# Performance work log

Hardware: AMD Instinct MI355X
Metric: run time of the kernel (lower is better)

Reference implementation:

```python
import jax, jax.numpy as jnp
import numpy as np
from jax import lax

DT = 0.1
V_DES = 12.64798288
T_HW = 0.50284384
A_MAX = 0.10033688
B_SAFE = 4.98937183
DELTA = 1.0
S0 = 0.13082412

B, S, I, H, K = 2048, 128, 8, 256, 50


def _lstm_layer(x, Wih, Whh, bih, bhh):
    # x: (B, S, in). PyTorch gate order: i, f, g, o. Fold both biases once.
    Bn = x.shape[0]
    Hd = Whh.shape[1]
    xg = jnp.einsum('bsi,gi->bsg', x, Wih) + bih + bhh  # (B, S, 4H)

    def step(carry, xg_t):
        h, c = carry
        g = xg_t + h @ Whh.T
        i, f, gg, o = jnp.split(g, 4, axis=-1)
        c = jax.nn.sigmoid(f) * c + jax.nn.sigmoid(i) * jnp.tanh(gg)
        h = jax.nn.sigmoid(o) * jnp.tanh(c)
        return (h, c), h

    init = (jnp.zeros((Bn, Hd), x.dtype), jnp.zeros((Bn, Hd), x.dtype))
    _, hs = lax.scan(step, init, jnp.swapaxes(xg, 0, 1))
    return jnp.swapaxes(hs, 0, 1)  # (B, S, H)


def _idm_rollout(v0, s_gap0, v_lead, horizon):
    sqrt_ab = float(np.sqrt(max(A_MAX, 1e-6) * max(B_SAFE, 1e-6)))

    def step(carry, _):
        v, s = carry
        dv = v_lead - v
        s_c = jnp.maximum(s, 1e-6)
        s_star = jnp.maximum(S0 + v * T_HW + v * dv / (2.0 * sqrt_ab + 1e-6), 0.0)
        acc = A_MAX * (1.0 - (v / V_DES) ** DELTA - (s_star / s_c) ** 2)
        v_next = jnp.maximum(v + DT * acc, 0.0)
        s_next = jnp.maximum(s + dv * DT, 1e-6)
        return (v_next, s_next), v_next

    _, vs = lax.scan(step, (v0, s_gap0), None, length=horizon)
    return jnp.swapaxes(vs, 0, 1)  # (B, K)


def setup_inputs() -> dict:
    key = jax.random.key(0)
    ks = jax.random.split(key, 14)
    sc = 0.05
    x = jax.random.uniform(ks[0], (B, S, I), jnp.float32) * 12.0  # speeds/features in [0, 12] m/s
    s_safe = 1.0 + jax.random.uniform(ks[1], (B,), jnp.float32) * 49.0  # gap in [1, 50] m
    v_lead = jax.random.uniform(ks[2], (B,), jnp.float32) * 12.0
    return {
        'x': x,
        's_safe_initial': s_safe,
        'v_lead_initial': v_lead,
        'Wih0': jax.random.normal(ks[3], (4 * H, I), jnp.float32) * sc,
        'Whh0': jax.random.normal(ks[4], (4 * H, H), jnp.float32) * sc,
        'bih0': jax.random.normal(ks[5], (4 * H,), jnp.float32) * sc,
        'bhh0': jax.random.normal(ks[6], (4 * H,), jnp.float32) * sc,
        'Wih1': jax.random.normal(ks[7], (4 * H, H), jnp.float32) * sc,
        'Whh1': jax.random.normal(ks[8], (4 * H, H), jnp.float32) * sc,
        'bih1': jax.random.normal(ks[9], (4 * H,), jnp.float32) * sc,
        'bhh1': jax.random.normal(ks[10], (4 * H,), jnp.float32) * sc,
        'Wfc': jax.random.normal(ks[11], (K, H), jnp.float32) * sc,
        'bfc': jax.random.normal(ks[12], (K,), jnp.float32) * sc,
    }


def reference(x, s_safe_initial, v_lead_initial, Wih0, Whh0, bih0, bhh0,
              Wih1, Whh1, bih1, bhh1, Wfc, bfc):
    h = _lstm_layer(x, Wih0, Whh0, bih0, bhh0)
    h = _lstm_layer(h, Wih1, Whh1, bih1, bhh1)
    y_lstm = h[:, -1, :] @ Wfc.T + bfc  # (B, K)
    y_idm = _idm_rollout(x[:, -1, 0], s_safe_initial, v_lead_initial, Wfc.shape[0])
    return (y_lstm, y_idm)
```

## Files before the change

kernel.cpp:

```cpp
#include <hip/hip_runtime.h>
#include <stdint.h>

typedef float f32x4 __attribute__((ext_vector_type(4)));
typedef unsigned int uint;
typedef unsigned long long ull;

#define NB 2048
#define NS 128
#define NI 8
#define NH 256
#define NG 1024
#define NK 50

#define A_SC 16.0f
#define W_SC 32.0f
#define INV_SC (1.0f/(A_SC*W_SC))

#define DT_    0.1f
#define V_DES_ 12.64798288f
#define T_HW_  0.50284384f
#define A_MAX_ 0.10033688f
#define B_SAFE_ 4.98937183f
#define S0_    0.13082412f

#define HADDR(row, boff) (((row) << 8) + (((((boff) >> 3) ^ ((row) & 15)) & 31) << 3) + ((boff) & 7))
#define GIDX(row, col) (((row) << 8) + ((col) ^ (((row) & 12) << 2)))

__device__ __forceinline__ uint8_t f2fp8(float v) {
    int r = __builtin_amdgcn_cvt_pk_fp8_f32(v, v, 0, false);
    return (uint8_t)(r & 0xff);
}
__device__ __forceinline__ float sigm(float x) { return 1.0f / (1.0f + __expf(-x)); }
__device__ __forceinline__ float tanh_f(float x) {
    x = fminf(fmaxf(x, -15.0f), 15.0f);
    float e = __expf(2.0f * x);
    return (e - 1.0f) / (e + 1.0f);
}

__global__ void k_pack(const float* __restrict__ W, uint8_t* __restrict__ out,
                       int tiles, int KB, int Nsrc, int Ksrc) {
    int gid = blockIdx.x * 256 + threadIdx.x;
    int total = tiles * KB * 64;
    if (gid >= total) return;
    int lane = gid & 63;
    int kb   = (gid >> 6) % KB;
    int tile = gid / (64 * KB);
    int n = tile * 16 + (lane & 15);
    int kbase = kb * 32 + (lane >> 4) * 8;
    uint64_t wbits = 0;
    #pragma unroll
    for (int j = 0; j < 8; ++j) {
        int k = kbase + j;
        float v = (n < Nsrc && k < Ksrc) ? W[(size_t)n * Ksrc + k] * W_SC : 0.0f;
        wbits |= ((uint64_t)f2fp8(v)) << (8 * j);
    }
    *(uint64_t*)(out + (size_t)gid * 8) = wbits;
}

__global__ void k_bias(const float* __restrict__ bih0, const float* __restrict__ bhh0,
                       const float* __restrict__ bih1, const float* __restrict__ bhh1,
                       float* __restrict__ b0, float* __restrict__ b1) {
    int i = blockIdx.x * 256 + threadIdx.x;
    if (i < NG) b0[i] = bih0[i] + bhh0[i];
    else if (i < 2 * NG) b1[i - NG] = bih1[i - NG] + bhh1[i - NG];
}

__global__ void k_x8(const float* __restrict__ x, uint8_t* __restrict__ x8) {
    int i = blockIdx.x * 256 + threadIdx.x;
    if (i < NB * NS * NI) x8[i] = f2fp8(x[i] * A_SC);
}

__global__ __launch_bounds__(512, 2)
void k_lstm3(const uint8_t* __restrict__ x8,
             const uint8_t* __restrict__ Wih0P, const uint8_t* __restrict__ Whh0P,
             const uint8_t* __restrict__ Wih1P, const uint8_t* __restrict__ Whh1P,
             const uint8_t* __restrict__ WfcP,
             const float* __restrict__ bias0, const float* __restrict__ bias1,
             const float* __restrict__ bfc,
             uint8_t* __restrict__ h0g, uint8_t* __restrict__ h1g,
             uint* __restrict__ ctrs, float* __restrict__ out) {
    __shared__ uint8_t h0st[8192];
    __shared__ uint8_t h1st[8192];
    __shared__ float gA[8192];
    __shared__ float gB[8192];

    const int tid  = threadIdx.x;
    const int w    = tid >> 6, lane = tid & 63;
    const int lrow = lane & 15, kgrp = lane >> 4;
    const int blk  = blockIdx.x;
    const int grp  = blk >> 2, slc = blk & 3;
    const int rowbase = grp * 32;
    const int g = w & 3, ub = w >> 1 & 0;
    const int ubk = w >> 2;

    long wI0[2], wH0[2][8], wI1[2][8], wH1[2][8];
    #pragma unroll
    for (int cc = 0; cc < 2; ++cc) {
        int T = g * 16 + slc * 4 + ubk * 2 + cc;
        wI0[cc] = *(const long*)(Wih0P + ((size_t)T * 64 + lane) * 8);
        #pragma unroll
        for (int kb = 0; kb < 8; ++kb) {
            wH0[cc][kb] = *(const long*)(Whh0P + (((size_t)T * 8 + kb) * 64 + lane) * 8);
            wI1[cc][kb] = *(const long*)(Wih1P + (((size_t)T * 8 + kb) * 64 + lane) * 8);
            wH1[cc][kb] = *(const long*)(Whh1P + (((size_t)T * 8 + kb) * 64 + lane) * 8);
        }
    }

    const int uu = tid & 63;
    const int rb = (tid >> 6) * 4;
    float bs0[4], bs1[4];
    #pragma unroll
    for (int q = 0; q < 4; ++q) {
        int n = q * 256 + slc * 64 + uu;
        bs0[q] = bias0[n]; bs1[q] = bias1[n];
    }
    float c0v[4] = {0,0,0,0}, c1v[4] = {0,0,0,0};

    { int4 z = {0,0,0,0}; ((int4*)h0st)[tid] = z; ((int4*)h1st)[tid] = z; }
    __syncthreads();

    uint8_t* const h0base = h0g + (size_t)grp * 16384;
    uint8_t* const h1base = h1g + (size_t)grp * 16384;
    uint* const myctr = ctrs + grp * 16;
    uint tgt = 0;

    for (int p = 0; p <= NS; ++p) {
        if (p < NS) {
            f32x4 acc[2][2];
            #pragma unroll
            for (int rr = 0; rr < 2; ++rr) { acc[rr][0] = (f32x4){0,0,0,0}; acc[rr][1] = (f32x4){0,0,0,0}; }
            #pragma unroll
            for (int rr = 0; rr < 2; ++rr) {
                long a0 = 0;
                if (kgrp == 0) a0 = *(const long*)(x8 + (size_t)(rowbase + rr * 16 + lrow) * (NS * NI) + p * 8);
                acc[rr][0] = __builtin_amdgcn_mfma_f32_16x16x32_fp8_fp8(a0, wI0[0], acc[rr][0], 0, 0, 0);
                acc[rr][1] = __builtin_amdgcn_mfma_f32_16x16x32_fp8_fp8(a0, wI0[1], acc[rr][1], 0, 0, 0);
                #pragma unroll
                for (int kb = 0; kb < 8; ++kb) {
                    long af = *(const long*)&h0st[HADDR(rr * 16 + lrow, kb * 32 + kgrp * 8)];
                    acc[rr][0] = __builtin_amdgcn_mfma_f32_16x16x32_fp8_fp8(af, wH0[0][kb], acc[rr][0], 0, 0, 0);
                    acc[rr][1] = __builtin_amdgcn_mfma_f32_16x16x32_fp8_fp8(af, wH0[1][kb], acc[rr][1], 0, 0, 0);
                }
            }
            #pragma unroll
            for (int rr = 0; rr < 2; ++rr)
            #pragma unroll
            for (int cc = 0; cc < 2; ++cc) {
                int colb = g * 64 + ubk * 32 + cc * 16 + lrow;
                #pragma unroll
                for (int r = 0; r < 4; ++r)
                    gA[GIDX(rr * 16 + kgrp * 4 + r, colb)] = acc[rr][cc][r];
            }
        }
        __syncthreads();

        if (p < NS) {
            uint8_t* dst = h0base + (size_t)(p & 1) * 8192;
            #pragma unroll
            for (int r = 0; r < 4; ++r) {
                int row = rb + r;
                float iv = gA[GIDX(row, uu)]       * INV_SC + bs0[0];
                float fv = gA[GIDX(row, 64 + uu)]  * INV_SC + bs0[1];
                float gv = gA[GIDX(row, 128 + uu)] * INV_SC + bs0[2];
                float ov = gA[GIDX(row, 192 + uu)] * INV_SC + bs0[3];
                float c = sigm(fv) * c0v[r] + sigm(iv) * tanh_f(gv);
                c0v[r] = c;
                float h = sigm(ov) * tanh_f(c);
                __hip_atomic_store(dst + row * 256 + slc * 64 + uu, f2fp8(h * A_SC),
                                   __ATOMIC_RELAXED, __HIP_MEMORY_SCOPE_AGENT);
            }
        }

        if (p >= 1) {
            f32x4 acc1[2][2];
            #pragma unroll
            for (int rr = 0; rr < 2; ++rr) { acc1[rr][0] = (f32x4){0,0,0,0}; acc1[rr][1] = (f32x4){0,0,0,0}; }
            #pragma unroll
            for (int rr = 0; rr < 2; ++rr) {
                #pragma unroll
                for (int kb = 0; kb < 8; ++kb) {
                    long af0 = *(const long*)&h0st[HADDR(rr * 16 + lrow, kb * 32 + kgrp * 8)];
                    acc1[rr][0] = __builtin_amdgcn_mfma_f32_16x16x32_fp8_fp8(af0, wI1[0][kb], acc1[rr][0], 0, 0, 0);
                    acc1[rr][1] = __builtin_amdgcn_mfma_f32_16x16x32_fp8_fp8(af0, wI1[1][kb], acc1[rr][1], 0, 0, 0);
                    long af1 = *(const long*)&h1st[HADDR(rr * 16 + lrow, kb * 32 + kgrp * 8)];
                    acc1[rr][0] = __builtin_amdgcn_mfma_f32_16x16x32_fp8_fp8(af1, wH1[0][kb], acc1[rr][0], 0, 0, 0);
                    acc1[rr][1] = __builtin_amdgcn_mfma_f32_16x16x32_fp8_fp8(af1, wH1[1][kb], acc1[rr][1], 0, 0, 0);
                }
            }
            #pragma unroll
            for (int rr = 0; rr < 2; ++rr)
            #pragma unroll
            for (int cc = 0; cc < 2; ++cc) {
                int colb = g * 64 + ubk * 32 + cc * 16 + lrow;
                #pragma unroll
                for (int r = 0; r < 4; ++r)
                    gB[GIDX(rr * 16 + kgrp * 4 + r, colb)] = acc1[rr][cc][r];
            }
        }
        __syncthreads();

        if (p >= 1) {
            uint8_t* dst = h1base + (size_t)((p - 1) & 1) * 8192;
            #pragma unroll
            for (int r = 0; r < 4; ++r) {
                int row = rb + r;
                float iv = gB[GIDX(row, uu)]       * INV_SC + bs1[0];
                float fv = gB[GIDX(row, 64 + uu)]  * INV_SC + bs1[1];
                float gv = gB[GIDX(row, 128 + uu)] * INV_SC + bs1[2];
                float ov = gB[GIDX(row, 192 + uu)] * INV_SC + bs1[3];
                float c = sigm(fv) * c1v[r] + sigm(iv) * tanh_f(gv);
                c1v[r] = c;
                float h = sigm(ov) * tanh_f(c);
                __hip_atomic_store(dst + row * 256 + slc * 64 + uu, f2fp8(h * A_SC),
                                   __ATOMIC_RELAXED, __HIP_MEMORY_SCOPE_AGENT);
            }
        }
        __syncthreads();

        tgt += 4;
        if (tid == 0) {
            __hip_atomic_fetch_add(myctr, 1u, __ATOMIC_RELAXED, __HIP_MEMORY_SCOPE_AGENT);
            int gd = 0;
            while (__hip_atomic_load(myctr, __ATOMIC_RELAXED, __HIP_MEMORY_SCOPE_AGENT) < tgt) {
                __builtin_amdgcn_s_sleep(1);
                if (++gd >= (1 << 22)) break;
            }
        }
        __syncthreads();

        {
            int rrow = tid & 31, seg = tid >> 5;
            const ull* s0p = (const ull*)(h0base + (size_t)(p & 1) * 8192 + rrow * 256 + seg * 16);
            const ull* s1p = (const ull*)(h1base + (size_t)((p + 1) & 1) * 8192 + rrow * 256 + seg * 16);
            #pragma unroll
            for (int j = 0; j < 2; ++j) {
                ull q0 = __hip_atomic_load(s0p + j, __ATOMIC_RELAXED, __HIP_MEMORY_SCOPE_AGENT);
                ull q1 = __hip_atomic_load(s1p + j, __ATOMIC_RELAXED, __HIP_MEMORY_SCOPE_AGENT);
                *(ull*)&h0st[HADDR(rrow, seg * 16 + j * 8)] = q0;
                *(ull*)&h1st[HADDR(rrow, seg * 16 + j * 8)] = q1;
            }
        }
        __syncthreads();
    }

    if (w < 2) {
        f32x4 a = (f32x4){0,0,0,0};
        #pragma unroll
        for (int kb = 0; kb < 8; ++kb) {
            long af = *(const long*)&h1st[HADDR(w * 16 + lrow, kb * 32 + kgrp * 8)];
            long bf = *(const long*)(WfcP + (((size_t)slc * 8 + kb) * 64 + lane) * 8);
            a = __builtin_amdgcn_mfma_f32_16x16x32_fp8_fp8(af, bf, a, 0, 0, 0);
        }
        int col = slc * 16 + lrow;
        if (col < NK) {
            float bb = bfc[col];
            #pragma unroll
            for (int r = 0; r < 4; ++r) {
                int row = rowbase + w * 16 + kgrp * 4 + r;
                out[(size_t)row * NK + col] = a[r] * INV_SC + bb;
            }
        }
    }
}

__global__ void k_idm(const float* __restrict__ x, const float* __restrict__ s0,
                      const float* __restrict__ vl, float* __restrict__ out) {
    int b = blockIdx.x * 256 + threadIdx.x;
    if (b >= NB) return;
    float v = x[(size_t)b * NS * NI + (NS - 1) * NI + 0];
    float s = s0[b];
    float vlead = vl[b];
    const float den = 2.0f * sqrtf(A_MAX_ * B_SAFE_) + 1e-6f;
    float* o = out + (size_t)NB * NK + (size_t)b * NK;
    #pragma unroll 1
    for (int k = 0; k < NK; ++k) {
        float dv = vlead - v;
        float sc = fmaxf(s, 1e-6f);
        float ss = fmaxf(S0_ + v * T_HW_ + v * dv / den, 0.0f);
        float a = A_MAX_ * (1.0f - v / V_DES_ - (ss / sc) * (ss / sc));
        v = fmaxf(v + DT_ * a, 0.0f);
        s = fmaxf(s + dv * DT_, 1e-6f);
        o[k] = v;
    }
}

extern "C" void kernel_launch(void* const* d_in, const int* in_sizes, int n_in,
                              void* d_out, int out_size, void* d_ws, size_t ws_size,
                              hipStream_t stream) {
    const float* x    = (const float*)d_in[0];
    const float* s0   = (const float*)d_in[1];
    const float* vl   = (const float*)d_in[2];
    const float* Wih0 = (const float*)d_in[3];
    const float* Whh0 = (const float*)d_in[4];
    const float* bih0 = (const float*)d_in[5];
    const float* bhh0 = (const float*)d_in[6];
    const float* Wih1 = (const float*)d_in[7];
    const float* Whh1 = (const float*)d_in[8];
    const float* bih1 = (const float*)d_in[9];
    const float* bhh1 = (const float*)d_in[10];
    const float* Wfc  = (const float*)d_in[11];
    const float* bfc  = (const float*)d_in[12];
    float* out = (float*)d_out;

    uint8_t* ws = (uint8_t*)d_ws;
    size_t off = 0;
    auto alloc = [&](size_t n) { uint8_t* p = ws + off; off += (n + 255) & ~(size_t)255; return p; };
    uint8_t* Wih0P = alloc(64 * 1 * 64 * 8);
    uint8_t* Whh0P = alloc(64 * 8 * 64 * 8);
    uint8_t* Wih1P = alloc(64 * 8 * 64 * 8);
    uint8_t* Whh1P = alloc(64 * 8 * 64 * 8);
    uint8_t* WfcP  = alloc(4 * 8 * 64 * 8);
    float* b0 = (float*)alloc(NG * 4);
    float* b1 = (float*)alloc(NG * 4);
    uint8_t* x8 = alloc((size_t)NB * NS * NI);
    uint8_t* h0g = alloc((size_t)64 * 16384);
    uint8_t* h1g = alloc((size_t)64 * 16384);
    uint*    ctrs = (uint*)alloc(64 * 64);
    size_t hz = (size_t)(((uint8_t*)ctrs + 64 * 64) - h0g);

    k_pack<<<(64 * 1 * 64 + 255) / 256, 256, 0, stream>>>(Wih0, Wih0P, 64, 1, NG, NI);
    k_pack<<<(64 * 8 * 64 + 255) / 256, 256, 0, stream>>>(Whh0, Whh0P, 64, 8, NG, NH);
    k_pack<<<(64 * 8 * 64 + 255) / 256, 256, 0, stream>>>(Wih1, Wih1P, 64, 8, NG, NH);
    k_pack<<<(64 * 8 * 64 + 255) / 256, 256, 0, stream>>>(Whh1, Whh1P, 64, 8, NG, NH);
    k_pack<<<(4 * 8 * 64 + 255) / 256, 256, 0, stream>>>(Wfc, WfcP, 4, 8, NK, NH);
    k_bias<<<(2 * NG + 255) / 256, 256, 0, stream>>>(bih0, bhh0, bih1, bhh1, b0, b1);
    k_x8<<<(NB * NS * NI + 255) / 256, 256, 0, stream>>>(x, x8);
    hipMemsetAsync(h0g, 0, hz, stream);

    void* kargs[] = { (void*)&x8, (void*)&Wih0P, (void*)&Whh0P, (void*)&Wih1P, (void*)&Whh1P,
                      (void*)&WfcP, (void*)&b0, (void*)&b1, (void*)&bfc,
                      (void*)&h0g, (void*)&h1g, (void*)&ctrs, (void*)&out };
    hipError_t ce = hipLaunchCooperativeKernel((const void*)k_lstm3, dim3(256), dim3(512), kargs, 0, stream);
    if (ce != hipSuccess) {
        k_lstm3<<<256, 512, 0, stream>>>(x8, Wih0P, Whh0P, Wih1P, Whh1P, WfcP, b0, b1, bfc, h0g, h1g, ctrs, out);
    }
    k_idm<<<(NB + 255) / 256, 256, 0, stream>>>(x, s0, vl, out);
}
```

Before: 924.1 us.

## Split each LSTM row group across eight blocks instead of four

Each 32-row batch group is now handled by 8 cooperating blocks, each owning 32 hidden units instead of 64. This halves per-block MFMA work, weight registers and gate LDS, and allows 4 blocks per CU with 512 total blocks. The bias is pre-scaled and folded into the accumulator store, and the gate stage packs two fp8 outputs per store. The cost is more blocks participating in each per-step counter barrier, and higher occupancy that may pressure registers.

```diff
diff --git a/kernel.cpp b/kernel.cpp
--- a/kernel.cpp
+++ b/kernel.cpp
@@ -4,6 +4,7 @@
 typedef float f32x4 __attribute__((ext_vector_type(4)));
 typedef unsigned int uint;
 typedef unsigned long long ull;
+typedef unsigned short ushort_t;
 
 #define NB 2048
 #define NS 128
@@ -14,6 +15,7 @@
 
 #define A_SC 16.0f
 #define W_SC 32.0f
+#define SC_PROD 512.0f
 #define INV_SC (1.0f/(A_SC*W_SC))
 
 #define DT_    0.1f
@@ -24,7 +26,7 @@
 #define S0_    0.13082412f
 
 #define HADDR(row, boff) (((row) << 8) + (((((boff) >> 3) ^ ((row) & 15)) & 31) << 3) + ((boff) & 7))
-#define GIDX(row, col) (((row) << 8) + ((col) ^ (((row) & 12) << 2)))
+#define GIDX(row, col) (((row) << 7) + ((col) ^ (((row) & 12) << 2)))
 
 __device__ __forceinline__ uint8_t f2fp8(float v) {
     int r = __builtin_amdgcn_cvt_pk_fp8_f32(v, v, 0, false);
@@ -61,8 +63,8 @@
                        const float* __restrict__ bih1, const float* __restrict__ bhh1,
                        float* __restrict__ b0, float* __restrict__ b1) {
     int i = blockIdx.x * 256 + threadIdx.x;
-    if (i < NG) b0[i] = bih0[i] + bhh0[i];
-    else if (i < 2 * NG) b1[i - NG] = bih1[i - NG] + bhh1[i - NG];
+    if (i < NG) b0[i] = (bih0[i] + bhh0[i]) * SC_PROD;
+    else if (i < 2 * NG) b1[i - NG] = (bih1[i - NG] + bhh1[i - NG]) * SC_PROD;
 }
 
 __global__ void k_x8(const float* __restrict__ x, uint8_t* __restrict__ x8) {
@@ -70,8 +72,8 @@
     if (i < NB * NS * NI) x8[i] = f2fp8(x[i] * A_SC);
 }
 
-__global__ __launch_bounds__(512, 2)
-void k_lstm3(const uint8_t* __restrict__ x8,
+__global__ __launch_bounds__(512, 4)
+void k_lstm4(const uint8_t* __restrict__ x8,
              const uint8_t* __restrict__ Wih0P, const uint8_t* __restrict__ Whh0P,
              const uint8_t* __restrict__ Wih1P, const uint8_t* __restrict__ Whh1P,
              const uint8_t* __restrict__ WfcP,
@@ -81,44 +83,43 @@
              uint* __restrict__ ctrs, float* __restrict__ out) {
     __shared__ uint8_t h0st[8192];
     __shared__ uint8_t h1st[8192];
-    __shared__ float gA[8192];
-    __shared__ float gB[8192];
+    __shared__ float gA[4096];
+    __shared__ float gB[4096];
 
     const int tid  = threadIdx.x;
     const int w    = tid >> 6, lane = tid & 63;
     const int lrow = lane & 15, kgrp = lane >> 4;
     const int blk  = blockIdx.x;
-    const int grp  = blk >> 2, slc = blk & 3;
+    const int grp  = blk >> 3, slc = blk & 7;
     const int rowbase = grp * 32;
-    const int g = w & 3, ub = w >> 1 & 0;
-    const int ubk = w >> 2;
-
-    long wI0[2], wH0[2][8], wI1[2][8], wH1[2][8];
+    const int g = w & 3, uh = w >> 2;
+    const int T = g * 16 + slc * 2 + uh;
+
+    long wI0, wH0[8], wI1[8], wH1[8];
+    wI0 = *(const long*)(Wih0P + ((size_t)T * 64 + lane) * 8);
     #pragma unroll
-    for (int cc = 0; cc < 2; ++cc) {
-        int T = g * 16 + slc * 4 + ubk * 2 + cc;
-        wI0[cc] = *(const long*)(Wih0P + ((size_t)T * 64 + lane) * 8);
-        #pragma unroll
-        for (int kb = 0; kb < 8; ++kb) {
-            wH0[cc][kb] = *(const long*)(Whh0P + (((size_t)T * 8 + kb) * 64 + lane) * 8);
-            wI1[cc][kb] = *(const long*)(Wih1P + (((size_t)T * 8 + kb) * 64 + lane) * 8);
-            wH1[cc][kb] = *(const long*)(Whh1P + (((size_t)T * 8 + kb) * 64 + lane) * 8);
-        }
-    }
-
-    const int uu = tid & 63;
-    const int rb = (tid >> 6) * 4;
-    float bs0[4], bs1[4];
+    for (int kb = 0; kb < 8; ++kb) {
+        wH0[kb] = *(const long*)(Whh0P + (((size_t)T * 8 + kb) * 64 + lane) * 8);
+        wI1[kb] = *(const long*)(Wih1P + (((size_t)T * 8 + kb) * 64 + lane) * 8);
+        wH1[kb] = *(const long*)(Whh1P + (((size_t)T * 8 + kb) * 64 + lane) * 8);
+    }
+    asm volatile("" : "+v"(wI0));
     #pragma unroll
-    for (int q = 0; q < 4; ++q) {
-        int n = q * 256 + slc * 64 + uu;
-        bs0[q] = bias0[n]; bs1[q] = bias1[n];
-    }
-    float c0v[4] = {0,0,0,0}, c1v[4] = {0,0,0,0};
+    for (int kb = 0; kb < 8; ++kb)
+        asm volatile("" : "+v"(wH0[kb]), "+v"(wI1[kb]), "+v"(wH1[kb]));
+
+    const int colw = g * 32 + uh * 16 + lrow;
+    const float bw0 = bias0[g * 256 + slc * 32 + uh * 16 + lrow];
+    const float bw1 = bias1[g * 256 + slc * 32 + uh * 16 + lrow];
+
+    const int nrow = tid >> 4;
+    const int nu2  = (tid & 15) * 2;
+    float c0v[2] = {0, 0}, c1v[2] = {0, 0};
 
     { int4 z = {0,0,0,0}; ((int4*)h0st)[tid] = z; ((int4*)h1st)[tid] = z; }
     __syncthreads();
 
+    const int abase = HADDR(lrow, kgrp * 8);
     uint8_t* const h0base = h0g + (size_t)grp * 16384;
     uint8_t* const h1base = h1g + (size_t)grp * 16384;
     uint* const myctr = ctrs + grp * 16;
@@ -126,98 +127,96 @@
 
     for (int p = 0; p <= NS; ++p) {
         if (p < NS) {
-            f32x4 acc[2][2];
-            #pragma unroll
-            for (int rr = 0; rr < 2; ++rr) { acc[rr][0] = (f32x4){0,0,0,0}; acc[rr][1] = (f32x4){0,0,0,0}; }
+            f32x4 acc[2];
+            acc[0] = (f32x4){0,0,0,0}; acc[1] = (f32x4){0,0,0,0};
             #pragma unroll
             for (int rr = 0; rr < 2; ++rr) {
                 long a0 = 0;
                 if (kgrp == 0) a0 = *(const long*)(x8 + (size_t)(rowbase + rr * 16 + lrow) * (NS * NI) + p * 8);
-                acc[rr][0] = __builtin_amdgcn_mfma_f32_16x16x32_fp8_fp8(a0, wI0[0], acc[rr][0], 0, 0, 0);
-                acc[rr][1] = __builtin_amdgcn_mfma_f32_16x16x32_fp8_fp8(a0, wI0[1], acc[rr][1], 0, 0, 0);
+                acc[rr] = __builtin_amdgcn_mfma_f32_16x16x32_fp8_fp8(a0, wI0, acc[rr], 0, 0, 0);
                 #pragma unroll
                 for (int kb = 0; kb < 8; ++kb) {
-                    long af = *(const long*)&h0st[HADDR(rr * 16 + lrow, kb * 32 + kgrp * 8)];
-                    acc[rr][0] = __builtin_amdgcn_mfma_f32_16x16x32_fp8_fp8(af, wH0[0][kb], acc[rr][0], 0, 0, 0);
-                    acc[rr][1] = __builtin_amdgcn_mfma_f32_16x16x32_fp8_fp8(af, wH0[1][kb], acc[rr][1], 0, 0, 0);
+                    long af = *(const long*)&h0st[(abase + rr * 4096) ^ (kb << 5)];
+                    acc[rr] = __builtin_amdgcn_mfma_f32_16x16x32_fp8_fp8(af, wH0[kb], acc[rr], 0, 0, 0);
                 }
             }
             #pragma unroll
             for (int rr = 0; rr < 2; ++rr)
             #pragma unroll
-            for (int cc = 0; cc < 2; ++cc) {
-                int colb = g * 64 + ubk * 32 + cc * 16 + lrow;
-                #pragma unroll
-                for (int r = 0; r < 4; ++r)
-                    gA[GIDX(rr * 16 + kgrp * 4 + r, colb)] = acc[rr][cc][r];
+            for (int r = 0; r < 4; ++r) {
+                int row = rr * 16 + kgrp * 4 + r;
+                gA[GIDX(row, colw)] = acc[rr][r] + bw0;
             }
         }
         __syncthreads();
 
         if (p < NS) {
-            uint8_t* dst = h0base + (size_t)(p & 1) * 8192;
-            #pragma unroll
-            for (int r = 0; r < 4; ++r) {
-                int row = rb + r;
-                float iv = gA[GIDX(row, uu)]       * INV_SC + bs0[0];
-                float fv = gA[GIDX(row, 64 + uu)]  * INV_SC + bs0[1];
-                float gv = gA[GIDX(row, 128 + uu)] * INV_SC + bs0[2];
-                float ov = gA[GIDX(row, 192 + uu)] * INV_SC + bs0[3];
-                float c = sigm(fv) * c0v[r] + sigm(iv) * tanh_f(gv);
-                c0v[r] = c;
-                float h = sigm(ov) * tanh_f(c);
-                __hip_atomic_store(dst + row * 256 + slc * 64 + uu, f2fp8(h * A_SC),
-                                   __ATOMIC_RELAXED, __HIP_MEMORY_SCOPE_AGENT);
-            }
+            float2 gq[4];
+            #pragma unroll
+            for (int q = 0; q < 4; ++q)
+                gq[q] = *(float2*)&gA[GIDX(nrow, q * 32 + nu2)];
+            float hh[2];
+            #pragma unroll
+            for (int u = 0; u < 2; ++u) {
+                float iv = ((u ? gq[0].y : gq[0].x)) * INV_SC;
+                float fv = ((u ? gq[1].y : gq[1].x)) * INV_SC;
+                float gv = ((u ? gq[2].y : gq[2].x)) * INV_SC;
+                float ov = ((u ? gq[3].y : gq[3].x)) * INV_SC;
+                float c = sigm(fv) * c0v[u] + sigm(iv) * tanh_f(gv);
+                c0v[u] = c;
+                hh[u] = sigm(ov) * tanh_f(c);
+            }
+            int pk = __builtin_amdgcn_cvt_pk_fp8_f32(hh[0] * A_SC, hh[1] * A_SC, 0, false);
+            __hip_atomic_store((ushort_t*)(h0base + (size_t)(p & 1) * 8192 + nrow * 256 + slc * 32 + nu2),
+                               (ushort_t)(pk & 0xffff), __ATOMIC_RELAXED, __HIP_MEMORY_SCOPE_AGENT);
         }
 
         if (p >= 1) {
-            f32x4 acc1[2][2];
-            #pragma unroll
-            for (int rr = 0; rr < 2; ++rr) { acc1[rr][0] = (f32x4){0,0,0,0}; acc1[rr][1] = (f32x4){0,0,0,0}; }
+            f32x4 acc[2];
+            acc[0] = (f32x4){0,0,0,0}; acc[1] = (f32x4){0,0,0,0};
             #pragma unroll
             for (int rr = 0; rr < 2; ++rr) {
                 #pragma unroll
                 for (int kb = 0; kb < 8; ++kb) {
-                    long af0 = *(const long*)&h0st[HADDR(rr * 16 + lrow, kb * 32 + kgrp * 8)];
-                    acc1[rr][0] = __builtin_amdgcn_mfma_f32_16x16x32_fp8_fp8(af0, wI1[0][kb], acc1[rr][0], 0, 0, 0);
-                    acc1[rr][1] = __builtin_amdgcn_mfma_f32_16x16x32_fp8_fp8(af0, wI1[1][kb], acc1[rr][1], 0, 0, 0);
-                    long af1 = *(const long*)&h1st[HADDR(rr * 16 + lrow, kb * 32 + kgrp * 8)];
-                    acc1[rr][0] = __builtin_amdgcn_mfma_f32_16x16x32_fp8_fp8(af1, wH1[0][kb], acc1[rr][0], 0, 0, 0);
-                    acc1[rr][1] = __builtin_amdgcn_mfma_f32_16x16x32_fp8_fp8(af1, wH1[1][kb], acc1[rr][1], 0, 0, 0);
+                    long af0 = *(const long*)&h0st[(abase + rr * 4096) ^ (kb << 5)];
+                    acc[rr] = __builtin_amdgcn_mfma_f32_16x16x32_fp8_fp8(af0, wI1[kb], acc[rr], 0, 0, 0);
+                    long af1 = *(const long*)&h1st[(abase + rr * 4096) ^ (kb << 5)];
+                    acc[rr] = __builtin_amdgcn_mfma_f32_16x16x32_fp8_fp8(af1, wH1[kb], acc[rr], 0, 0, 0);
                 }
             }
             #pragma unroll
             for (int rr = 0; rr < 2; ++rr)
             #pragma unroll
-            for (int cc = 0; cc < 2; ++cc) {
-                int colb = g * 64 + ubk * 32 + cc * 16 + lrow;
-                #pragma unroll
-                for (int r = 0; r < 4; ++r)
-                    gB[GIDX(rr * 16 + kgrp * 4 + r, colb)] = acc1[rr][cc][r];
+            for (int r = 0; r < 4; ++r) {
+                int row = rr * 16 + kgrp * 4 + r;
+                gB[GIDX(row, colw)] = acc[rr][r] + bw1;
             }
         }
         __syncthreads();
 
         if (p >= 1) {
-            uint8_t* dst = h1base + (size_t)((p - 1) & 1) * 8192;
-            #pragma unroll
-            for (int r = 0; r < 4; ++r) {
-                int row = rb + r;
-                float iv = gB[GIDX(row, uu)]       * INV_SC + bs1[0];
-                float fv = gB[GIDX(row, 64 + uu)]  * INV_SC + bs1[1];
-                float gv = gB[GIDX(row, 128 + uu)] * INV_SC + bs1[2];
-                float ov = gB[GIDX(row, 192 + uu)] * INV_SC + bs1[3];
-                float c = sigm(fv) * c1v[r] + sigm(iv) * tanh_f(gv);
-                c1v[r] = c;
-                float h = sigm(ov) * tanh_f(c);
-                __hip_atomic_store(dst + row * 256 + slc * 64 + uu, f2fp8(h * A_SC),
-                                   __ATOMIC_RELAXED, __HIP_MEMORY_SCOPE_AGENT);
-            }
-        }
-        __syncthreads();
-
-        tgt += 4;
+            float2 gq[4];
+            #pragma unroll
+            for (int q = 0; q < 4; ++q)
+                gq[q] = *(float2*)&gB[GIDX(nrow, q * 32 + nu2)];
+            float hh[2];
+            #pragma unroll
+            for (int u = 0; u < 2; ++u) {
+                float iv = ((u ? gq[0].y : gq[0].x)) * INV_SC;
+                float fv = ((u ? gq[1].y : gq[1].x)) * INV_SC;
+                float gv = ((u ? gq[2].y : gq[2].x)) * INV_SC;
+                float ov = ((u ? gq[3].y : gq[3].x)) * INV_SC;
+                float c = sigm(fv) * c1v[u] + sigm(iv) * tanh_f(gv);
+                c1v[u] = c;
+                hh[u] = sigm(ov) * tanh_f(c);
+            }
+            int pk = __builtin_amdgcn_cvt_pk_fp8_f32(hh[0] * A_SC, hh[1] * A_SC, 0, false);
+            __hip_atomic_store((ushort_t*)(h1base + (size_t)((p - 1) & 1) * 8192 + nrow * 256 + slc * 32 + nu2),
+                               (ushort_t)(pk & 0xffff), __ATOMIC_RELAXED, __HIP_MEMORY_SCOPE_AGENT);
+        }
+        __syncthreads();
+
+        tgt += 8;
         if (tid == 0) {
             __hip_atomic_fetch_add(myctr, 1u, __ATOMIC_RELAXED, __HIP_MEMORY_SCOPE_AGENT);
             int gd = 0;
@@ -243,7 +242,7 @@
         __syncthreads();
     }
 
-    if (w < 2) {
+    if (slc < 4 && w < 2) {
         f32x4 a = (f32x4){0,0,0,0};
         #pragma unroll
         for (int kb = 0; kb < 8; ++kb) {
@@ -330,9 +329,9 @@
     void* kargs[] = { (void*)&x8, (void*)&Wih0P, (void*)&Whh0P, (void*)&Wih1P, (void*)&Whh1P,
                       (void*)&WfcP, (void*)&b0, (void*)&b1, (void*)&bfc,
                       (void*)&h0g, (void*)&h1g, (void*)&ctrs, (void*)&out };
-    hipError_t ce = hipLaunchCooperativeKernel((const void*)k_lstm3, dim3(256), dim3(512), kargs, 0, stream);
+    hipError_t ce = hipLaunchCooperativeKernel((const void*)k_lstm4, dim3(512), dim3(512), kargs, 0, stream);
     if (ce != hipSuccess) {
-        k_lstm3<<<256, 512, 0, stream>>>(x8, Wih0P, Whh0P, Wih1P, Whh1P, WfcP, b0, b1, bfc, h0g, h1g, ctrs, out);
+        k_lstm4<<<512, 512, 0, stream>>>(x8, Wih0P, Whh0P, Wih1P, Whh1P, WfcP, b0, b1, bfc, h0g, h1g, ctrs, out);
     }
     k_idm<<<(NB + 255) / 256, 256, 0, stream>>>(x, s0, vl, out);
 }
```

New measurement: 1.051 ms. 13.7% more time.

## Split per-layer inter-block counters and overlap layer-1 hidden exchange with compute

Applied to the files above, without the earlier changes.

Replaces the single end-of-step counter barrier with separate counters for layer-0 and layer-1 hidden states, so each block waits only for the data it needs and the layer-1 exchange is prefetched at the start of the next step. It also vectorises the gate epilogue (float4 reads, packed fp8 stores of four units), uses 16-byte LDS reads with a new swizzle, folds the pre-scaled bias into the accumulator writeback, and pins weights in AGPRs via inline asm. The intent is to cut inter-block synchronisation latency and LDS/global traffic on each recurrent step, at the cost of more complex ordering that could introduce races.

```diff
diff --git a/kernel.cpp b/kernel.cpp
--- a/kernel.cpp
+++ b/kernel.cpp
@@ -2,6 +2,7 @@
 #include <stdint.h>
 
 typedef float f32x4 __attribute__((ext_vector_type(4)));
+typedef long long2_t __attribute__((ext_vector_type(2)));
 typedef unsigned int uint;
 typedef unsigned long long ull;
 
@@ -14,7 +15,8 @@
 
 #define A_SC 16.0f
 #define W_SC 32.0f
-#define INV_SC (1.0f/(A_SC*W_SC))
+#define SC_PROD 512.0f
+#define INV_SC (1.0f/512.0f)
 
 #define DT_    0.1f
 #define V_DES_ 12.64798288f
@@ -23,7 +25,7 @@
 #define B_SAFE_ 4.98937183f
 #define S0_    0.13082412f
 
-#define HADDR(row, boff) (((row) << 8) + (((((boff) >> 3) ^ ((row) & 15)) & 31) << 3) + ((boff) & 7))
+#define HADDR16(row, boff) (((row) << 8) + (((((boff) >> 4) ^ ((row) & 15)) & 15) << 4) + ((boff) & 15))
 #define GIDX(row, col) (((row) << 8) + ((col) ^ (((row) & 12) << 2)))
 
 __device__ __forceinline__ uint8_t f2fp8(float v) {
@@ -61,8 +63,8 @@
                        const float* __restrict__ bih1, const float* __restrict__ bhh1,
                        float* __restrict__ b0, float* __restrict__ b1) {
     int i = blockIdx.x * 256 + threadIdx.x;
-    if (i < NG) b0[i] = bih0[i] + bhh0[i];
-    else if (i < 2 * NG) b1[i - NG] = bih1[i - NG] + bhh1[i - NG];
+    if (i < NG) b0[i] = (bih0[i] + bhh0[i]) * SC_PROD;
+    else if (i < 2 * NG) b1[i - NG] = (bih1[i - NG] + bhh1[i - NG]) * SC_PROD;
 }
 
 __global__ void k_x8(const float* __restrict__ x, uint8_t* __restrict__ x8) {
@@ -71,7 +73,7 @@
 }
 
 __global__ __launch_bounds__(512, 2)
-void k_lstm3(const uint8_t* __restrict__ x8,
+void k_lstm6(const uint8_t* __restrict__ x8,
              const uint8_t* __restrict__ Wih0P, const uint8_t* __restrict__ Whh0P,
              const uint8_t* __restrict__ Wih1P, const uint8_t* __restrict__ Whh1P,
              const uint8_t* __restrict__ WfcP,
@@ -85,13 +87,11 @@
     __shared__ float gB[8192];
 
     const int tid  = threadIdx.x;
-    const int w    = tid >> 6, lane = tid & 63;
+    const int lane = tid & 63, w = tid >> 6;
     const int lrow = lane & 15, kgrp = lane >> 4;
-    const int blk  = blockIdx.x;
-    const int grp  = blk >> 2, slc = blk & 3;
+    const int grp  = blockIdx.x >> 2, slc = blockIdx.x & 3;
     const int rowbase = grp * 32;
-    const int g = w & 3, ub = w >> 1 & 0;
-    const int ubk = w >> 2;
+    const int g = w & 3, ubk = w >> 2;
 
     long wI0[2], wH0[2][8], wI1[2][8], wH1[2][8];
     #pragma unroll
@@ -105,162 +105,212 @@
             wH1[cc][kb] = *(const long*)(Whh1P + (((size_t)T * 8 + kb) * 64 + lane) * 8);
         }
     }
-
-    const int uu = tid & 63;
-    const int rb = (tid >> 6) * 4;
-    float bs0[4], bs1[4];
     #pragma unroll
-    for (int q = 0; q < 4; ++q) {
-        int n = q * 256 + slc * 64 + uu;
-        bs0[q] = bias0[n]; bs1[q] = bias1[n];
-    }
+    for (int cc = 0; cc < 2; ++cc) {
+        asm volatile("" : "+a"(wI0[cc]));
+        #pragma unroll
+        for (int kb = 0; kb < 8; ++kb)
+            asm volatile("" : "+a"(wH0[cc][kb]), "+a"(wI1[cc][kb]), "+a"(wH1[cc][kb]));
+    }
+
+    float bw0[2], bw1[2];
+    #pragma unroll
+    for (int cc = 0; cc < 2; ++cc) {
+        int n = g * 256 + slc * 64 + ubk * 32 + cc * 16 + lrow;
+        bw0[cc] = bias0[n]; bw1[cc] = bias1[n];
+    }
+
+    const int nrow = tid >> 4;
+    const int ub4  = (tid & 15) * 4;
     float c0v[4] = {0,0,0,0}, c1v[4] = {0,0,0,0};
 
     { int4 z = {0,0,0,0}; ((int4*)h0st)[tid] = z; ((int4*)h1st)[tid] = z; }
     __syncthreads();
 
-    uint8_t* const h0base = h0g + (size_t)grp * 16384;
-    uint8_t* const h1base = h1g + (size_t)grp * 16384;
-    uint* const myctr = ctrs + grp * 16;
-    uint tgt = 0;
+    uint8_t* const h0gg = h0g + (size_t)grp * 16384;
+    uint8_t* const h1gg = h1g + (size_t)grp * 16384;
+    uint* const ctr0 = ctrs + grp * 32;
+    uint* const ctr1 = ctrs + grp * 32 + 16;
+    uint t0 = 0, t1 = 0;
+
+    const int rrow = tid & 31, seg = tid >> 5;
+    const int rkb = seg >> 1, rkg = (seg & 1) << 1;
+    const int rboff0 = rkg * 64 + rkb * 8, rboff1 = (rkg + 1) * 64 + rkb * 8;
+
+#define WAITC(CP, TGT) do { \
+    if (tid == 0) { \
+        uint gd_ = 0; \
+        while (__hip_atomic_load((CP), __ATOMIC_RELAXED, __HIP_MEMORY_SCOPE_AGENT) < (TGT)) { \
+            __builtin_amdgcn_s_sleep(1); \
+            if (++gd_ > (1u << 24)) break; \
+        } \
+    } \
+    __syncthreads(); \
+} while (0)
 
     for (int p = 0; p <= NS; ++p) {
+        ull pr0 = 0, pr1 = 0;
+        if (p >= 2) {
+            WAITC(ctr1, t1);
+            const uint8_t* s = h1gg + (size_t)(p & 1) * 8192 + rrow * 256 + seg * 16;
+            pr0 = __hip_atomic_load((const ull*)s,       __ATOMIC_RELAXED, __HIP_MEMORY_SCOPE_AGENT);
+            pr1 = __hip_atomic_load((const ull*)(s + 8), __ATOMIC_RELAXED, __HIP_MEMORY_SCOPE_AGENT);
+        }
+
         if (p < NS) {
             f32x4 acc[2][2];
             #pragma unroll
             for (int rr = 0; rr < 2; ++rr) { acc[rr][0] = (f32x4){0,0,0,0}; acc[rr][1] = (f32x4){0,0,0,0}; }
             #pragma unroll
             for (int rr = 0; rr < 2; ++rr) {
-                long a0 = 0;
-                if (kgrp == 0) a0 = *(const long*)(x8 + (size_t)(rowbase + rr * 16 + lrow) * (NS * NI) + p * 8);
-                acc[rr][0] = __builtin_amdgcn_mfma_f32_16x16x32_fp8_fp8(a0, wI0[0], acc[rr][0], 0, 0, 0);
-                acc[rr][1] = __builtin_amdgcn_mfma_f32_16x16x32_fp8_fp8(a0, wI0[1], acc[rr][1], 0, 0, 0);
+                long ax = 0;
+                if (kgrp == 0) ax = *(const long*)(x8 + (size_t)(rowbase + rr * 16 + lrow) * (NS * NI) + p * 8);
+                acc[rr][0] = __builtin_amdgcn_mfma_f32_16x16x32_fp8_fp8(ax, wI0[0], acc[rr][0], 0, 0, 0);
+                acc[rr][1] = __builtin_amdgcn_mfma_f32_16x16x32_fp8_fp8(ax, wI0[1], acc[rr][1], 0, 0, 0);
                 #pragma unroll
-                for (int kb = 0; kb < 8; ++kb) {
-                    long af = *(const long*)&h0st[HADDR(rr * 16 + lrow, kb * 32 + kgrp * 8)];
-                    acc[rr][0] = __builtin_amdgcn_mfma_f32_16x16x32_fp8_fp8(af, wH0[0][kb], acc[rr][0], 0, 0, 0);
-                    acc[rr][1] = __builtin_amdgcn_mfma_f32_16x16x32_fp8_fp8(af, wH0[1][kb], acc[rr][1], 0, 0, 0);
+                for (int kbh = 0; kbh < 4; ++kbh) {
+                    const int gsw = ((((kgrp << 2) + kbh) ^ lrow) & 15) << 4;
+                    long2_t q = *(const long2_t*)&h0st[((rr * 16 + lrow) << 8) + gsw];
+                    acc[rr][0] = __builtin_amdgcn_mfma_f32_16x16x32_fp8_fp8(q.x, wH0[0][2*kbh],   acc[rr][0], 0, 0, 0);
+                    acc[rr][0] = __builtin_amdgcn_mfma_f32_16x16x32_fp8_fp8(q.y, wH0[0][2*kbh+1], acc[rr][0], 0, 0, 0);
+                    acc[rr][1] = __builtin_amdgcn_mfma_f32_16x16x32_fp8_fp8(q.x, wH0[1][2*kbh],   acc[rr][1], 0, 0, 0);
+                    acc[rr][1] = __builtin_amdgcn_mfma_f32_16x16x32_fp8_fp8(q.y, wH0[1][2*kbh+1], acc[rr][1], 0, 0, 0);
                 }
             }
             #pragma unroll
             for (int rr = 0; rr < 2; ++rr)
             #pragma unroll
             for (int cc = 0; cc < 2; ++cc) {
-                int colb = g * 64 + ubk * 32 + cc * 16 + lrow;
+                const int colw = g * 64 + ubk * 32 + cc * 16 + lrow;
                 #pragma unroll
                 for (int r = 0; r < 4; ++r)
-                    gA[GIDX(rr * 16 + kgrp * 4 + r, colb)] = acc[rr][cc][r];
+                    gA[GIDX(rr * 16 + kgrp * 4 + r, colw)] = acc[rr][cc][r] + bw0[cc];
             }
         }
         __syncthreads();
 
         if (p < NS) {
-            uint8_t* dst = h0base + (size_t)(p & 1) * 8192;
-            #pragma unroll
-            for (int r = 0; r < 4; ++r) {
-                int row = rb + r;
-                float iv = gA[GIDX(row, uu)]       * INV_SC + bs0[0];
-                float fv = gA[GIDX(row, 64 + uu)]  * INV_SC + bs0[1];
-                float gv = gA[GIDX(row, 128 + uu)] * INV_SC + bs0[2];
-                float ov = gA[GIDX(row, 192 + uu)] * INV_SC + bs0[3];
-                float c = sigm(fv) * c0v[r] + sigm(iv) * tanh_f(gv);
-                c0v[r] = c;
-                float h = sigm(ov) * tanh_f(c);
-                __hip_atomic_store(dst + row * 256 + slc * 64 + uu, f2fp8(h * A_SC),
-                                   __ATOMIC_RELAXED, __HIP_MEMORY_SCOPE_AGENT);
-            }
-        }
+            float4 q0 = *(float4*)&gA[GIDX(nrow, ub4)];
+            float4 q1 = *(float4*)&gA[GIDX(nrow, 64 + ub4)];
+            float4 q2 = *(float4*)&gA[GIDX(nrow, 128 + ub4)];
+            float4 q3 = *(float4*)&gA[GIDX(nrow, 192 + ub4)];
+            float hh[4];
+            #pragma unroll
+            for (int u = 0; u < 4; ++u) {
+                float iv = (&q0.x)[u] * INV_SC, fv = (&q1.x)[u] * INV_SC;
+                float gv = (&q2.x)[u] * INV_SC, ov = (&q3.x)[u] * INV_SC;
+                float c = sigm(fv) * c0v[u] + sigm(iv) * tanh_f(gv);
+                c0v[u] = c;
+                hh[u] = sigm(ov) * tanh_f(c) * A_SC;
+            }
+            int pk = __builtin_amdgcn_cvt_pk_fp8_f32(hh[0], hh[1], 0, false);
+            pk = __builtin_amdgcn_cvt_pk_fp8_f32(hh[2], hh[3], pk, true);
+            __hip_atomic_store((uint*)(h0gg + (size_t)(p & 1) * 8192 + nrow * 256 + slc * 64 + ub4),
+                               (uint)pk, __ATOMIC_RELAXED, __HIP_MEMORY_SCOPE_AGENT);
+        }
+        if (p >= 2) {
+            *(ull*)&h1st[HADDR16(rrow, rboff0)] = pr0;
+            *(ull*)&h1st[HADDR16(rrow, rboff1)] = pr1;
+        }
+        __syncthreads();
+        if (p < NS) { if (tid == 0) __hip_atomic_fetch_add(ctr0, 1u, __ATOMIC_RELAXED, __HIP_MEMORY_SCOPE_AGENT); t0 += 4; }
 
         if (p >= 1) {
-            f32x4 acc1[2][2];
-            #pragma unroll
-            for (int rr = 0; rr < 2; ++rr) { acc1[rr][0] = (f32x4){0,0,0,0}; acc1[rr][1] = (f32x4){0,0,0,0}; }
+            f32x4 acc[2][2];
+            #pragma unroll
+            for (int rr = 0; rr < 2; ++rr) { acc[rr][0] = (f32x4){0,0,0,0}; acc[rr][1] = (f32x4){0,0,0,0}; }
             #pragma unroll
             for (int rr = 0; rr < 2; ++rr) {
                 #pragma unroll
-                for (int kb = 0; kb < 8; ++kb) {
-                    long af0 = *(const long*)&h0st[HADDR(rr * 16 + lrow, kb * 32 + kgrp * 8)];
-                    acc1[rr][0] = __builtin_amdgcn_mfma_f32_16x16x32_fp8_fp8(af0, wI1[0][kb], acc1[rr][0], 0, 0, 0);
-                    acc1[rr][1] = __builtin_amdgcn_mfma_f32_16x16x32_fp8_fp8(af0, wI1[1][kb], acc1[rr][1], 0, 0, 0);
-                    long af1 = *(const long*)&h1st[HADDR(rr * 16 + lrow, kb * 32 + kgrp * 8)];
-                    acc1[rr][0] = __builtin_amdgcn_mfma_f32_16x16x32_fp8_fp8(af1, wH1[0][kb], acc1[rr][0], 0, 0, 0);
-                    acc1[rr][1] = __builtin_amdgcn_mfma_f32_16x16x32_fp8_fp8(af1, wH1[1][kb], acc1[rr][1], 0, 0, 0);
+                for (int kbh = 0; kbh < 4; ++kbh) {
+                    const int gsw = ((((kgrp << 2) + kbh) ^ lrow) & 15) << 4;
+                    long2_t q = *(const long2_t*)&h0st[((rr * 16 + lrow) << 8) + gsw];
+                    long2_t r2 = *(const long2_t*)&h1st[((rr * 16 + lrow) << 8) + gsw];
+                    acc[rr][0] = __builtin_amdgcn_mfma_f32_16x16x32_fp8_fp8(q.x,  wI1[0][2*kbh],   acc[rr][0], 0, 0, 0);
+                    acc[rr][0] = __builtin_amdgcn_mfma_f32_16x16x32_fp8_fp8(q.y,  wI1[0][2*kbh+1], acc[rr][0], 0, 0, 0);
+                    acc[rr][0] = __builtin_amdgcn_mfma_f32_16x16x32_fp8_fp8(r2.x, wH1[0][2*kbh],   acc[rr][0], 0, 0, 0);
+                    acc[rr][0] = __builtin_amdgcn_mfma_f32_16x16x32_fp8_fp8(r2.y, wH1[0][2*kbh+1], acc[rr][0], 0, 0, 0);
+                    acc[rr][1] = __builtin_amdgcn_mfma_f32_16x16x32_fp8_fp8(q.x,  wI1[1][2*kbh],   acc[rr][1], 0, 0, 0);
+                    acc[rr][1] = __builtin_amdgcn_mfma_f32_16x16x32_fp8_fp8(q.y,  wI1[1][2*kbh+1], acc[rr][1], 0, 0, 0);
+                    acc[rr][1] = __builtin_amdgcn_mfma_f32_16x16x32_fp8_fp8(r2.x, wH1[1][2*kbh],   acc[rr][1], 0, 0, 0);
+                    acc[rr][1] = __builtin_amdgcn_mfma_f32_16x16x32_fp8_fp8(r2.y, wH1[1][2*kbh+1], acc[rr][1], 0, 0, 0);
                 }
             }
             #pragma unroll
             for (int rr = 0; rr < 2; ++rr)
             #pragma unroll
             for (int cc = 0; cc < 2; ++cc) {
-                int colb = g * 64 + ubk * 32 + cc * 16 + lrow;
+                const int colw = g * 64 + ubk * 32 + cc * 16 + lrow;
                 #pragma unroll
                 for (int r = 0; r < 4; ++r)
-                    gB[GIDX(rr * 16 + kgrp * 4 + r, colb)] = acc1[rr][cc][r];
+                    gB[GIDX(rr * 16 + kgrp * 4 + r, colw)] = acc[rr][cc][r] + bw1[cc];
             }
         }
         __syncthreads();
 
         if (p >= 1) {
-            uint8_t* dst = h1base + (size_t)((p - 1) & 1) * 8192;
-            #pragma unroll
-            for (int r = 0; r < 4; ++r) {
-                int row = rb + r;
-                float iv = gB[GIDX(row, uu)]       * INV_SC + bs1[0];
-                float fv = gB[GIDX(row, 64 + uu)]  * INV_SC + bs1[1];
-                float gv = gB[GIDX(row, 128 + uu)] * INV_SC + bs1[2];
-                float ov = gB[GIDX(row, 192 + uu)] * INV_SC + bs1[3];
-                float c = sigm(fv) * c1v[r] + sigm(iv) * tanh_f(gv);
-                c1v[r] = c;
-                float h = sigm(ov) * tanh_f(c);
-                __hip_atomic_store(dst + row * 256 + slc * 64 + uu, f2fp8(h * A_SC),
-                                   __ATOMIC_RELAXED, __HIP_MEMORY_SCOPE_AGENT);
-            }
-        }
-        __syncthreads();
-
-        tgt += 4;
-        if (tid == 0) {
-            __hip_atomic_fetch_add(myctr, 1u, __ATOMIC_RELAXED, __HIP_MEMORY_SCOPE_AGENT);
-            int gd = 0;
-            while (__hip_atomic_load(myctr, __ATOMIC_RELAXED, __HIP_MEMORY_SCOPE_AGENT) < tgt) {
-                __builtin_amdgcn_s_sleep(1);
-                if (++gd >= (1 << 22)) break;
-            }
-        }
-        __syncthreads();
-
-        {
-            int rrow = tid & 31, seg = tid >> 5;
-            const ull* s0p = (const ull*)(h0base + (size_t)(p & 1) * 8192 + rrow * 256 + seg * 16);
-            const ull* s1p = (const ull*)(h1base + (size_t)((p + 1) & 1) * 8192 + rrow * 256 + seg * 16);
-            #pragma unroll
-            for (int j = 0; j < 2; ++j) {
-                ull q0 = __hip_atomic_load(s0p + j, __ATOMIC_RELAXED, __HIP_MEMORY_SCOPE_AGENT);
-                ull q1 = __hip_atomic_load(s1p + j, __ATOMIC_RELAXED, __HIP_MEMORY_SCOPE_AGENT);
-                *(ull*)&h0st[HADDR(rrow, seg * 16 + j * 8)] = q0;
-                *(ull*)&h1st[HADDR(rrow, seg * 16 + j * 8)] = q1;
-            }
-        }
-        __syncthreads();
-    }
+            float4 q0 = *(float4*)&gB[GIDX(nrow, ub4)];
+            float4 q1 = *(float4*)&gB[GIDX(nrow, 64 + ub4)];
+            float4 q2 = *(float4*)&gB[GIDX(nrow, 128 + ub4)];
+            float4 q3 = *(float4*)&gB[GIDX(nrow, 192 + ub4)];
+            float hh[4];
+            #pragma unroll
+            for (int u = 0; u < 4; ++u) {
+                float iv = (&q0.x)[u] * INV_SC, fv = (&q1.x)[u] * INV_SC;
+                float gv = (&q2.x)[u] * INV_SC, ov = (&q3.x)[u] * INV_SC;
+                float c = sigm(fv) * c1v[u] + sigm(iv) * tanh_f(gv);
+                c1v[u] = c;
+                hh[u] = sigm(ov) * tanh_f(c) * A_SC;
+            }
+            int pk = __builtin_amdgcn_cvt_pk_fp8_f32(hh[0], hh[1], 0, false);
+            pk = __builtin_amdgcn_cvt_pk_fp8_f32(hh[2], hh[3], pk, true);
+            __hip_atomic_store((uint*)(h1gg + (size_t)((p + 1) & 1) * 8192 + nrow * 256 + slc * 64 + ub4),
+                               (uint)pk, __ATOMIC_RELAXED, __HIP_MEMORY_SCOPE_AGENT);
+        }
+        __syncthreads();
+        if (p >= 1) { if (tid == 0) __hip_atomic_fetch_add(ctr1, 1u, __ATOMIC_RELAXED, __HIP_MEMORY_SCOPE_AGENT); t1 += 4; }
+
+        if (p < NS) {
+            WAITC(ctr0, t0);
+            const uint8_t* s = h0gg + (size_t)(p & 1) * 8192 + rrow * 256 + seg * 16;
+            ull a0 = __hip_atomic_load((const ull*)s,       __ATOMIC_RELAXED, __HIP_MEMORY_SCOPE_AGENT);
+            ull a1 = __hip_atomic_load((const ull*)(s + 8), __ATOMIC_RELAXED, __HIP_MEMORY_SCOPE_AGENT);
+            *(ull*)&h0st[HADDR16(rrow, rboff0)] = a0;
+            *(ull*)&h0st[HADDR16(rrow, rboff1)] = a1;
+        }
+        __syncthreads();
+    }
+
+    {
+        WAITC(ctr1, t1);
+        const uint8_t* s = h1gg + (size_t)8192 + rrow * 256 + seg * 16;
+        ull a0 = __hip_atomic_load((const ull*)s,       __ATOMIC_RELAXED, __HIP_MEMORY_SCOPE_AGENT);
+        ull a1 = __hip_atomic_load((const ull*)(s + 8), __ATOMIC_RELAXED, __HIP_MEMORY_SCOPE_AGENT);
+        *(ull*)&h1st[HADDR16(rrow, rboff0)] = a0;
+        *(ull*)&h1st[HADDR16(rrow, rboff1)] = a1;
+    }
+    __syncthreads();
 
     if (w < 2) {
-        f32x4 a = (f32x4){0,0,0,0};
+        f32x4 a = {0,0,0,0};
         #pragma unroll
-        for (int kb = 0; kb < 8; ++kb) {
-            long af = *(const long*)&h1st[HADDR(w * 16 + lrow, kb * 32 + kgrp * 8)];
-            long bf = *(const long*)(WfcP + (((size_t)slc * 8 + kb) * 64 + lane) * 8);
-            a = __builtin_amdgcn_mfma_f32_16x16x32_fp8_fp8(af, bf, a, 0, 0, 0);
-        }
-        int col = slc * 16 + lrow;
+        for (int kbh = 0; kbh < 4; ++kbh) {
+            const int gsw = ((((kgrp << 2) + kbh) ^ lrow) & 15) << 4;
+            long2_t q = *(const long2_t*)&h1st[((w * 16 + lrow) << 8) + gsw];
+            long b0_ = *(const long*)(WfcP + (((size_t)slc * 8 + 2 * kbh) * 64 + lane) * 8);
+            long b1_ = *(const long*)(WfcP + (((size_t)slc * 8 + 2 * kbh + 1) * 64 + lane) * 8);
+            a = __builtin_amdgcn_mfma_f32_16x16x32_fp8_fp8(q.x, b0_, a, 0, 0, 0);
+            a = __builtin_amdgcn_mfma_f32_16x16x32_fp8_fp8(q.y, b1_, a, 0, 0, 0);
+        }
+        const int col = slc * 16 + lrow;
         if (col < NK) {
             float bb = bfc[col];
             #pragma unroll
-            for (int r = 0; r < 4; ++r) {
-                int row = rowbase + w * 16 + kgrp * 4 + r;
-                out[(size_t)row * NK + col] = a[r] * INV_SC + bb;
-            }
-        }
-    }
+            for (int r = 0; r < 4; ++r)
+                out[(size_t)(rowbase + w * 16 + kgrp * 4 + r) * NK + col] = a[r] * INV_SC + bb;
+        }
+    }
+#undef WAITC
 }
 
 __global__ void k_idm(const float* __restrict__ x, const float* __restrict__ s0,
@@ -315,8 +365,8 @@
     uint8_t* x8 = alloc((size_t)NB * NS * NI);
     uint8_t* h0g = alloc((size_t)64 * 16384);
     uint8_t* h1g = alloc((size_t)64 * 16384);
-    uint*    ctrs = (uint*)alloc(64 * 64);
-    size_t hz = (size_t)(((uint8_t*)ctrs + 64 * 64) - h0g);
+    uint*    ctrs = (uint*)alloc(64 * 32 * 4);
+    size_t hz = (size_t)(((uint8_t*)ctrs + 64 * 32 * 4) - h0g);
 
     k_pack<<<(64 * 1 * 64 + 255) / 256, 256, 0, stream>>>(Wih0, Wih0P, 64, 1, NG, NI);
     k_pack<<<(64 * 8 * 64 + 255) / 256, 256, 0, stream>>>(Whh0, Whh0P, 64, 8, NG, NH);
@@ -330,9 +380,9 @@
     void* kargs[] = { (void*)&x8, (void*)&Wih0P, (void*)&Whh0P, (void*)&Wih1P, (void*)&Whh1P,
                       (void*)&WfcP, (void*)&b0, (void*)&b1, (void*)&bfc,
                       (void*)&h0g, (void*)&h1g, (void*)&ctrs, (void*)&out };
-    hipError_t ce = hipLaunchCooperativeKernel((const void*)k_lstm3, dim3(256), dim3(512), kargs, 0, stream);
+    hipError_t ce = hipLaunchCooperativeKernel((const void*)k_lstm6, dim3(256), dim3(512), kargs, 0, stream);
     if (ce != hipSuccess) {
-        k_lstm3<<<256, 512, 0, stream>>>(x8, Wih0P, Whh0P, Wih1P, Whh1P, WfcP, b0, b1, bfc, h0g, h1g, ctrs, out);
+        k_lstm6<<<256, 512, 0, stream>>>(x8, Wih0P, Whh0P, Wih1P, Whh1P, WfcP, b0, b1, bfc, h0g, h1g, ctrs, out);
     }
     k_idm<<<(NB + 255) / 256, 256, 0, stream>>>(x, s0, vl, out);
 }
```

Measured after the change: 1.035 ms. 12.0% more time.
